# Kernel optimization log

Hardware: AMD Instinct MI355X
Metric: run time of the kernel (lower is better)

The kernel has to match this reference:

```python
import jax, jax.numpy as jnp
import numpy as np

N_QUBITS = 10
DIM = 2 ** N_QUBITS
W_MUL = (2.0 ** 0.5) * (5.0 ** -0.5)  # he_std with gain=sqrt(2), use_wscale=True, lrmul=1
_X = jnp.array([[0.0, 1.0], [1.0, 0.0]], dtype=jnp.complex64)
_XX = jnp.kron(_X, _X)  # 4x4
_I4 = jnp.eye(4, dtype=jnp.complex64)


def _ry(theta):
    c = jnp.cos(theta / 2)
    s = jnp.sin(theta / 2)
    return jnp.stack([jnp.stack([c, -s]), jnp.stack([s, c])]).astype(jnp.complex64)


def _rxx(theta):
    c = jnp.cos(theta / 2).astype(jnp.complex64)
    s = jnp.sin(theta / 2).astype(jnp.complex64)
    return c * _I4 - 1j * s * _XX


def _apply_1q(M, g, q):
    # left-multiply kron-expanded 1-qubit gate on qubit q (qubit 0 = most significant)
    Mr = M.reshape((2,) * N_QUBITS + (DIM,))
    Mr = jnp.tensordot(g, Mr, axes=((1,), (q,)))
    Mr = jnp.moveaxis(Mr, 0, q)
    return Mr.reshape(DIM, DIM)


def _apply_2q(M, g4, q1, q2):
    g = g4.reshape(2, 2, 2, 2)
    Mr = M.reshape((2,) * N_QUBITS + (DIM,))
    Mr = jnp.tensordot(g, Mr, axes=((2, 3), (q1, q2)))
    Mr = jnp.moveaxis(Mr, (0, 1), (q1, q2))
    return Mr.reshape(DIM, DIM)


def _circuit_unitary(weight):
    w = weight * W_MUL
    U = jnp.eye(DIM, dtype=jnp.complex64)
    for q in range(0, N_QUBITS, 2):
        U = _apply_1q(U, _ry(w[0]), q)
        U = _apply_1q(U, _ry(w[1]), q + 1)
        U = _apply_2q(U, _rxx(w[2]), q, q + 1)
        U = _apply_1q(U, _ry(w[3]), q)
        U = _apply_1q(U, _ry(w[4]), q + 1)
        U = _apply_2q(U, _rxx(w[5]), q, q + 1)
    return U


def setup_inputs() -> dict:
    key = jax.random.key(0)
    k1, k2 = jax.random.split(key)
    x = jax.random.normal(k1, (8, DIM, DIM), dtype=jnp.float32)
    weight = jax.random.uniform(k2, (6,), dtype=jnp.float32, minval=0.0, maxval=2.0 * np.pi)
    return {"x": x, "weight": weight}


def reference(x, weight):
    U = _circuit_unitary(weight)
    xc = x.astype(jnp.complex64)
    # forward: dag(U) @ x @ U  (broadcast over batch)
    out = jnp.matmul(jnp.matmul(U.conj().T, xc), U)
    # return real/imag stacked so output is real-dtype
    return jnp.stack([out.real, out.imag])
```

## Files before the change

kernel.cpp:

```cpp
#include <hip/hip_runtime.h>
#include <hip/hip_fp16.h>

#define DIM 1024
#define NB 8
#define CBLK 8
#define LSTRIDE 9

__device__ __forceinline__ int lidx(int r, int c) {
  return r * LSTRIDE + c;
}

__device__ __forceinline__ unsigned rflu(unsigned x) {
  return (unsigned)__builtin_amdgcn_readfirstlane((int)x);
}
__device__ __forceinline__ unsigned h2u(__half2 h) {
  union { __half2 h; unsigned u; } c; c.h = h; return c.u;
}
__device__ __forceinline__ __half2 u2h(unsigned u) {
  union { unsigned u; __half2 h; } c; c.u = u; return c.h;
}
__device__ __forceinline__ __half2 h2swap(__half2 x) {
  unsigned u = h2u(x);
  return u2h((u >> 16) | (u << 16));
}

struct __align__(16) H2x4 { __half2 h[4]; };

__device__ __forceinline__ void mv4p(__half2* v, const int stride,
                                     const unsigned (&Wre2)[4][4],
                                     const unsigned (&Wimn)[4][4]) {
  __half2 x0 = v[0], x1 = v[stride], x2 = v[2 * stride], x3 = v[3 * stride];
  __half2 s0 = h2swap(x0), s1 = h2swap(x1), s2 = h2swap(x2), s3 = h2swap(x3);
  #pragma unroll
  for (int p = 0; p < 4; ++p) {
    __half2 a = u2h(Wre2[p][0]) * x0;
    a = __hfma2(u2h(Wimn[p][0]), s0, a);
    a = __hfma2(u2h(Wre2[p][2]), x2, a);
    a = __hfma2(u2h(Wimn[p][2]), s2, a);
    __half2 b = u2h(Wre2[p][1]) * x1;
    b = __hfma2(u2h(Wimn[p][1]), s1, b);
    b = __hfma2(u2h(Wre2[p][3]), x3, b);
    b = __hfma2(u2h(Wimn[p][3]), s3, b);
    v[p * stride] = a + b;
  }
}

__device__ __forceinline__ void mv4rp(const __half2* x, __half2* y,
                                      const unsigned (&Wri)[4][4]) {
  #pragma unroll
  for (int p = 0; p < 4; ++p) {
    __half2 a = u2h(Wri[p][0]) * x[0];
    a = __hfma2(u2h(Wri[p][2]), x[2], a);
    __half2 b = u2h(Wri[p][1]) * x[1];
    b = __hfma2(u2h(Wri[p][3]), x[3], b);
    y[p] = a + b;
  }
}

__device__ void compute_W(const float* __restrict__ wgt, int pass,
                          unsigned (&Wre2)[4][4], unsigned (&Wimn)[4][4],
                          unsigned (&Wri)[4][4]) {
  const float WMUL = 0.6324555320336759f;
  float ca[6], sa[6];
  #pragma unroll
  for (int i = 0; i < 6; ++i) {
    float h = wgt[i] * (0.5f * WMUL);
    ca[i] = cosf(h);
    sa[i] = sinf(h);
  }
  float R01[4][4], R34[4][4];
  {
    float a0[2][2] = {{ca[0], -sa[0]}, {sa[0], ca[0]}};
    float b0[2][2] = {{ca[1], -sa[1]}, {sa[1], ca[1]}};
    float a1[2][2] = {{ca[3], -sa[3]}, {sa[3], ca[3]}};
    float b1[2][2] = {{ca[4], -sa[4]}, {sa[4], ca[4]}};
    #pragma unroll
    for (int i = 0; i < 4; ++i)
      #pragma unroll
      for (int j = 0; j < 4; ++j) {
        R01[i][j] = a0[i >> 1][j >> 1] * b0[i & 1][j & 1];
        R34[i][j] = a1[i >> 1][j >> 1] * b1[i & 1][j & 1];
      }
  }
  float M2re[4][4], M2im[4][4];
  #pragma unroll
  for (int k = 0; k < 4; ++k)
    #pragma unroll
    for (int j = 0; j < 4; ++j) {
      M2re[k][j] = ca[2] * R01[k][j];
      M2im[k][j] = -sa[2] * R01[3 - k][j];
    }
  float M3re[4][4], M3im[4][4];
  #pragma unroll
  for (int i = 0; i < 4; ++i)
    #pragma unroll
    for (int j = 0; j < 4; ++j) {
      float rr = 0.f, ii = 0.f;
      #pragma unroll
      for (int k = 0; k < 4; ++k) {
        rr += R34[i][k] * M2re[k][j];
        ii += R34[i][k] * M2im[k][j];
      }
      M3re[i][j] = rr;
      M3im[i][j] = ii;
    }
  #pragma unroll
  for (int k = 0; k < 4; ++k)
    #pragma unroll
    for (int j = 0; j < 4; ++j) {
      float vre = ca[5] * M3re[k][j] + sa[5] * M3im[3 - k][j];
      float vim = ca[5] * M3im[k][j] - sa[5] * M3re[3 - k][j];
      float wim = (pass == 0) ? -vim : vim;
      Wre2[j][k] = rflu(h2u(__floats2half2_rn(vre, vre)));
      Wimn[j][k] = rflu(h2u(__floats2half2_rn(-wim, wim)));
      Wri[j][k] = rflu(h2u(__floats2half2_rn(vre, wim)));
    }
}

template <int PASS>
__global__ __launch_bounds__(512, 4) void qpass(const void* __restrict__ srcv,
                                                const float* __restrict__ weight,
                                                void* __restrict__ dstv,
                                                int batch0) {
  __shared__ __half2 tile[DIM * LSTRIDE];
  const int t = threadIdx.x;

  int B = blockIdx.x;
  int total = gridDim.x;
  int L;
  if ((total & 7) == 0) {
    int q = total >> 3;
    L = (B & 7) * q + (B >> 3);
  } else {
    L = B;
  }
  const int cg = L & 127;
  const int bl = L >> 7;
  const int bg = batch0 + bl;
  const int c0 = cg * CBLK;

  unsigned Wre2[4][4], Wimn[4][4], Wri[4][4];
  compute_W(weight, PASS, Wre2, Wimn, Wri);

  if (PASS == 0) {
    const float* s = (const float*)srcv + (size_t)bg * DIM * DIM + c0;
    #pragma unroll
    for (int it = 0; it < 4; ++it) {
      int u = it * 512 + t;
      int r = u >> 1, h = (u & 1) * 4;
      float4 v = *reinterpret_cast<const float4*>(s + (size_t)r * DIM + h);
      tile[lidx(r, h + 0)] = __half2half2(__float2half(v.x));
      tile[lidx(r, h + 1)] = __half2half2(__float2half(v.y));
      tile[lidx(r, h + 2)] = __half2half2(__float2half(v.z));
      tile[lidx(r, h + 3)] = __half2half2(__float2half(v.w));
    }
  } else {
    const __half2* s = (const __half2*)srcv + ((size_t)bl << 20) + c0;
    #pragma unroll
    for (int it = 0; it < 4; ++it) {
      int u = it * 512 + t;
      int r = u >> 1, h = (u & 1) * 4;
      H2x4 v = *reinterpret_cast<const H2x4*>(s + (size_t)r * DIM + h);
      tile[lidx(r, h + 0)] = v.h[0];
      tile[lidx(r, h + 1)] = v.h[1];
      tile[lidx(r, h + 2)] = v.h[2];
      tile[lidx(r, h + 3)] = v.h[3];
    }
  }
  __syncthreads();

  {
    int c = t & 7, g = t >> 3;
    __half2 v[16];
    if (PASS == 0) {
      #pragma unroll
      for (int k0 = 0; k0 < 4; ++k0) {
        __half2 xs[4];
        #pragma unroll
        for (int k1 = 0; k1 < 4; ++k1)
          xs[k1] = tile[lidx(g + k0 * 256 + k1 * 64, c)];
        mv4rp(xs, &v[k0 * 4], Wri);
      }
    } else {
      #pragma unroll
      for (int k0 = 0; k0 < 4; ++k0)
        #pragma unroll
        for (int k1 = 0; k1 < 4; ++k1)
          v[k0 * 4 + k1] = tile[lidx(g + k0 * 256 + k1 * 64, c)];
      #pragma unroll
      for (int k0 = 0; k0 < 4; ++k0) mv4p(&v[k0 * 4], 1, Wre2, Wimn);
    }
    #pragma unroll
    for (int k1 = 0; k1 < 4; ++k1) mv4p(&v[k1], 4, Wre2, Wimn);
    #pragma unroll
    for (int k0 = 0; k0 < 4; ++k0)
      #pragma unroll
      for (int k1 = 0; k1 < 4; ++k1)
        tile[lidx(g + k0 * 256 + k1 * 64, c)] = v[k0 * 4 + k1];
  }
  __syncthreads();

  {
    int c = t & 7, g = t >> 3;
    int base = (g >> 2) * 64 + (g & 3);
    __half2 v[16];
    #pragma unroll
    for (int k2 = 0; k2 < 4; ++k2)
      #pragma unroll
      for (int k3 = 0; k3 < 4; ++k3)
        v[k2 * 4 + k3] = tile[lidx(base + k2 * 16 + k3 * 4, c)];
    #pragma unroll
    for (int k2 = 0; k2 < 4; ++k2) mv4p(&v[k2 * 4], 1, Wre2, Wimn);
    #pragma unroll
    for (int k3 = 0; k3 < 4; ++k3) mv4p(&v[k3], 4, Wre2, Wimn);
    #pragma unroll
    for (int k2 = 0; k2 < 4; ++k2)
      #pragma unroll
      for (int k3 = 0; k3 < 4; ++k3)
        tile[lidx(base + k2 * 16 + k3 * 4, c)] = v[k2 * 4 + k3];
  }
  __syncthreads();

  #pragma unroll
  for (int it = 0; it < 4; ++it) {
    int c = t & 7;
    int g = (t >> 3) + 64 * it;
    __half2 v[4];
    #pragma unroll
    for (int k = 0; k < 4; ++k) v[k] = tile[lidx(4 * g + k, c)];
    mv4p(v, 1, Wre2, Wimn);
    if (PASS == 0) {
      __half2* d = (__half2*)dstv + ((size_t)bl << 20) + (size_t)(c0 + c) * DIM + 4 * g;
      H2x4 o;
      o.h[0] = v[0]; o.h[1] = v[1]; o.h[2] = v[2]; o.h[3] = v[3];
      *reinterpret_cast<H2x4*>(d) = o;
    } else {
      float2 f0 = __half22float2(v[0]), f1 = __half22float2(v[1]);
      float2 f2 = __half22float2(v[2]), f3 = __half22float2(v[3]);
      float* dr = (float*)dstv + ((size_t)bg << 20) + (size_t)(c0 + c) * DIM + 4 * g;
      float* di = dr + ((size_t)1 << 23);
      *reinterpret_cast<float4*>(dr) = make_float4(f0.x, f1.x, f2.x, f3.x);
      *reinterpret_cast<float4*>(di) = make_float4(f0.y, f1.y, f2.y, f3.y);
    }
  }
}

extern "C" void kernel_launch(void* const* d_in, const int* in_sizes, int n_in,
                              void* d_out, int out_size, void* d_ws, size_t ws_size,
                              hipStream_t stream) {
  const float* x = (const float*)d_in[0];
  const float* w = (const float*)d_in[1];

  const size_t per_batch = (size_t)DIM * DIM * sizeof(__half2);
  int max_nb = (int)(ws_size / per_batch);
  if (max_nb > NB) max_nb = NB;
  if (max_nb < 1) max_nb = 1;

  for (int b0 = 0; b0 < NB; b0 += max_nb) {
    int nb = NB - b0 < max_nb ? NB - b0 : max_nb;
    dim3 grid(128 * nb);
    qpass<0><<<grid, 512, 0, stream>>>(x, w, d_ws, b0);
    qpass<1><<<grid, 512, 0, stream>>>(d_ws, w, d_out, b0);
  }
}
```

Baseline: 55.33 us.

## Fuse first gate layer into global load and restructure LDS gate stages

Applies the first 4x4 gate layer directly in registers on the values just loaded from global memory. This removes one LDS round trip. The remaining four gate layers are regrouped into two stages of 16 registers each, and the output is written as 64-byte contiguous chunks per thread with nontemporal stores for the final fp32 output. The LDS row stride changes from 9 to 10, which alters bank-conflict behaviour and the shared-memory footprint and may affect occupancy.

```diff
diff --git a/kernel.cpp b/kernel.cpp
--- a/kernel.cpp
+++ b/kernel.cpp
@@ -4,7 +4,9 @@
 #define DIM 1024
 #define NB 8
 #define CBLK 8
-#define LSTRIDE 9
+#define LSTRIDE 10
+
+typedef float vfloat4 __attribute__((ext_vector_type(4)));
 
 __device__ __forceinline__ int lidx(int r, int c) {
   return r * LSTRIDE + c;
@@ -142,105 +144,108 @@
   unsigned Wre2[4][4], Wimn[4][4], Wri[4][4];
   compute_W(weight, PASS, Wre2, Wimn, Wri);
 
-  if (PASS == 0) {
-    const float* s = (const float*)srcv + (size_t)bg * DIM * DIM + c0;
-    #pragma unroll
-    for (int it = 0; it < 4; ++it) {
-      int u = it * 512 + t;
-      int r = u >> 1, h = (u & 1) * 4;
-      float4 v = *reinterpret_cast<const float4*>(s + (size_t)r * DIM + h);
-      tile[lidx(r, h + 0)] = __half2half2(__float2half(v.x));
-      tile[lidx(r, h + 1)] = __half2half2(__float2half(v.y));
-      tile[lidx(r, h + 2)] = __half2half2(__float2half(v.z));
-      tile[lidx(r, h + 3)] = __half2half2(__float2half(v.w));
-    }
-  } else {
-    const __half2* s = (const __half2*)srcv + ((size_t)bl << 20) + c0;
-    #pragma unroll
-    for (int it = 0; it < 4; ++it) {
-      int u = it * 512 + t;
-      int r = u >> 1, h = (u & 1) * 4;
-      H2x4 v = *reinterpret_cast<const H2x4*>(s + (size_t)r * DIM + h);
-      tile[lidx(r, h + 0)] = v.h[0];
-      tile[lidx(r, h + 1)] = v.h[1];
-      tile[lidx(r, h + 2)] = v.h[2];
-      tile[lidx(r, h + 3)] = v.h[3];
-    }
+  {
+    const int r0 = t >> 1, h = (t & 1) * 4;
+    __half2 o[4][4];
+    if (PASS == 0) {
+      const float* s = (const float*)srcv + (size_t)bg * DIM * DIM + c0 + h;
+      float4 ld[4];
+      #pragma unroll
+      for (int k = 0; k < 4; ++k)
+        ld[k] = *reinterpret_cast<const float4*>(s + (size_t)(r0 + 256 * k) * DIM);
+      __half2 xh[4][4];
+      #pragma unroll
+      for (int k = 0; k < 4; ++k) {
+        xh[k][0] = __half2half2(__float2half(ld[k].x));
+        xh[k][1] = __half2half2(__float2half(ld[k].y));
+        xh[k][2] = __half2half2(__float2half(ld[k].z));
+        xh[k][3] = __half2half2(__float2half(ld[k].w));
+      }
+      #pragma unroll
+      for (int j = 0; j < 4; ++j) {
+        __half2 x[4] = {xh[0][j], xh[1][j], xh[2][j], xh[3][j]};
+        __half2 y[4];
+        mv4rp(x, y, Wri);
+        #pragma unroll
+        for (int p = 0; p < 4; ++p) o[p][j] = y[p];
+      }
+    } else {
+      const __half2* s = (const __half2*)srcv + ((size_t)bl << 20) + c0 + h;
+      H2x4 ld[4];
+      #pragma unroll
+      for (int k = 0; k < 4; ++k)
+        ld[k] = *reinterpret_cast<const H2x4*>(s + (size_t)(r0 + 256 * k) * DIM);
+      #pragma unroll
+      for (int j = 0; j < 4; ++j) {
+        __half2 x[4] = {ld[0].h[j], ld[1].h[j], ld[2].h[j], ld[3].h[j]};
+        mv4p(x, 1, Wre2, Wimn);
+        #pragma unroll
+        for (int p = 0; p < 4; ++p) o[p][j] = x[p];
+      }
+    }
+    #pragma unroll
+    for (int p = 0; p < 4; ++p)
+      #pragma unroll
+      for (int j = 0; j < 4; ++j)
+        tile[lidx(r0 + 256 * p, h + j)] = o[p][j];
   }
   __syncthreads();
 
   {
-    int c = t & 7, g = t >> 3;
+    int c = t & 7, gg = t >> 3;
+    int base = (gg >> 4) * 256 + (gg & 15);
     __half2 v[16];
+    #pragma unroll
+    for (int k1 = 0; k1 < 4; ++k1)
+      #pragma unroll
+      for (int k2 = 0; k2 < 4; ++k2)
+        v[k1 * 4 + k2] = tile[lidx(base + k1 * 64 + k2 * 16, c)];
+    #pragma unroll
+    for (int k1 = 0; k1 < 4; ++k1) mv4p(&v[k1 * 4], 1, Wre2, Wimn);
+    #pragma unroll
+    for (int k2 = 0; k2 < 4; ++k2) mv4p(&v[k2], 4, Wre2, Wimn);
+    #pragma unroll
+    for (int k1 = 0; k1 < 4; ++k1)
+      #pragma unroll
+      for (int k2 = 0; k2 < 4; ++k2)
+        tile[lidx(base + k1 * 64 + k2 * 16, c)] = v[k1 * 4 + k2];
+  }
+  __syncthreads();
+
+  {
+    int c = t & 7, q = t >> 3;
+    __half2 v[16];
+    #pragma unroll
+    for (int k = 0; k < 16; ++k) v[k] = tile[lidx(16 * q + k, c)];
+    #pragma unroll
+    for (int k3 = 0; k3 < 4; ++k3) mv4p(&v[4 * k3], 1, Wre2, Wimn);
+    #pragma unroll
+    for (int k4 = 0; k4 < 4; ++k4) mv4p(&v[k4], 4, Wre2, Wimn);
     if (PASS == 0) {
-      #pragma unroll
-      for (int k0 = 0; k0 < 4; ++k0) {
-        __half2 xs[4];
-        #pragma unroll
-        for (int k1 = 0; k1 < 4; ++k1)
-          xs[k1] = tile[lidx(g + k0 * 256 + k1 * 64, c)];
-        mv4rp(xs, &v[k0 * 4], Wri);
+      __half2* d = (__half2*)dstv + ((size_t)bl << 20) + (size_t)(c0 + c) * DIM + 16 * q;
+      #pragma unroll
+      for (int g4 = 0; g4 < 4; ++g4) {
+        H2x4 o;
+        o.h[0] = v[4 * g4 + 0];
+        o.h[1] = v[4 * g4 + 1];
+        o.h[2] = v[4 * g4 + 2];
+        o.h[3] = v[4 * g4 + 3];
+        *reinterpret_cast<H2x4*>(d + 4 * g4) = o;
       }
     } else {
-      #pragma unroll
-      for (int k0 = 0; k0 < 4; ++k0)
-        #pragma unroll
-        for (int k1 = 0; k1 < 4; ++k1)
-          v[k0 * 4 + k1] = tile[lidx(g + k0 * 256 + k1 * 64, c)];
-      #pragma unroll
-      for (int k0 = 0; k0 < 4; ++k0) mv4p(&v[k0 * 4], 1, Wre2, Wimn);
-    }
-    #pragma unroll
-    for (int k1 = 0; k1 < 4; ++k1) mv4p(&v[k1], 4, Wre2, Wimn);
-    #pragma unroll
-    for (int k0 = 0; k0 < 4; ++k0)
-      #pragma unroll
-      for (int k1 = 0; k1 < 4; ++k1)
-        tile[lidx(g + k0 * 256 + k1 * 64, c)] = v[k0 * 4 + k1];
-  }
-  __syncthreads();
-
-  {
-    int c = t & 7, g = t >> 3;
-    int base = (g >> 2) * 64 + (g & 3);
-    __half2 v[16];
-    #pragma unroll
-    for (int k2 = 0; k2 < 4; ++k2)
-      #pragma unroll
-      for (int k3 = 0; k3 < 4; ++k3)
-        v[k2 * 4 + k3] = tile[lidx(base + k2 * 16 + k3 * 4, c)];
-    #pragma unroll
-    for (int k2 = 0; k2 < 4; ++k2) mv4p(&v[k2 * 4], 1, Wre2, Wimn);
-    #pragma unroll
-    for (int k3 = 0; k3 < 4; ++k3) mv4p(&v[k3], 4, Wre2, Wimn);
-    #pragma unroll
-    for (int k2 = 0; k2 < 4; ++k2)
-      #pragma unroll
-      for (int k3 = 0; k3 < 4; ++k3)
-        tile[lidx(base + k2 * 16 + k3 * 4, c)] = v[k2 * 4 + k3];
-  }
-  __syncthreads();
-
-  #pragma unroll
-  for (int it = 0; it < 4; ++it) {
-    int c = t & 7;
-    int g = (t >> 3) + 64 * it;
-    __half2 v[4];
-    #pragma unroll
-    for (int k = 0; k < 4; ++k) v[k] = tile[lidx(4 * g + k, c)];
-    mv4p(v, 1, Wre2, Wimn);
-    if (PASS == 0) {
-      __half2* d = (__half2*)dstv + ((size_t)bl << 20) + (size_t)(c0 + c) * DIM + 4 * g;
-      H2x4 o;
-      o.h[0] = v[0]; o.h[1] = v[1]; o.h[2] = v[2]; o.h[3] = v[3];
-      *reinterpret_cast<H2x4*>(d) = o;
-    } else {
-      float2 f0 = __half22float2(v[0]), f1 = __half22float2(v[1]);
-      float2 f2 = __half22float2(v[2]), f3 = __half22float2(v[3]);
-      float* dr = (float*)dstv + ((size_t)bg << 20) + (size_t)(c0 + c) * DIM + 4 * g;
+      float* dr = (float*)dstv + ((size_t)bg << 20) + (size_t)(c0 + c) * DIM + 16 * q;
       float* di = dr + ((size_t)1 << 23);
-      *reinterpret_cast<float4*>(dr) = make_float4(f0.x, f1.x, f2.x, f3.x);
-      *reinterpret_cast<float4*>(di) = make_float4(f0.y, f1.y, f2.y, f3.y);
+      #pragma unroll
+      for (int g4 = 0; g4 < 4; ++g4) {
+        float2 f0 = __half22float2(v[4 * g4 + 0]);
+        float2 f1 = __half22float2(v[4 * g4 + 1]);
+        float2 f2 = __half22float2(v[4 * g4 + 2]);
+        float2 f3 = __half22float2(v[4 * g4 + 3]);
+        vfloat4 re = {f0.x, f1.x, f2.x, f3.x};
+        vfloat4 im = {f0.y, f1.y, f2.y, f3.y};
+        __builtin_nontemporal_store(re, reinterpret_cast<vfloat4*>(dr + 4 * g4));
+        __builtin_nontemporal_store(im, reinterpret_cast<vfloat4*>(di + 4 * g4));
+      }
     }
   }
 }
```

Measured after the change: 138.2 us. 150% more time.
